# Optimization experiments

Hardware: AMD Instinct MI355X
Metric: run time of the kernel (lower is better)

The kernel has to match this reference:

```python
import jax, jax.numpy as jnp
import numpy as np

B, C3, H3, W3 = 8, 512, 24, 24
C5, H5, W5 = 256, 96, 96
GRIDS = (6, 3, 2, 1)
GROUPS = 2


def conv2d(x, w):
    # stride-1 'same' conv (matches torch autopad k//2 for odd k), NCHW/OIHW
    return jax.lax.conv_general_dilated(x, w, (1, 1), 'SAME',
                                        dimension_numbers=('NCHW', 'OIHW', 'NCHW'))


def conv_bn_silu(x, w):
    # ultralytics-style Conv = Conv2d(bias=False) + BatchNorm2d + SiLU.
    # BN in eval with default running stats (mean=0, var=1, gamma=1, beta=0) is identity.
    return jax.nn.silu(conv2d(x, w))


def psp(x):
    # adaptive_avg_pool2d to (g, g) for each grid; H,W divisible by all grids -> equal bins
    b, c, h, w = x.shape
    outs = []
    for g in GRIDS:
        outs.append(x.reshape(b, c, g, h // g, g, w // g).mean(axis=(3, 5)).reshape(b, c, g * g))
    return jnp.concatenate(outs, axis=2)  # [b, c, 36+9+4+1=50]


def resize_bilinear_ac(x, oh, ow):
    # F.interpolate(mode='bilinear', align_corners=True)
    n, c, h, w = x.shape
    ys = jnp.linspace(0.0, h - 1.0, oh)
    xs = jnp.linspace(0.0, w - 1.0, ow)
    y0 = jnp.clip(jnp.floor(ys).astype(jnp.int32), 0, h - 2)
    x0 = jnp.clip(jnp.floor(xs).astype(jnp.int32), 0, w - 2)
    wy = (ys - y0)[None, None, :, None]
    wx = (xs - x0)[None, None, None, :]
    xr = jnp.take(x, y0, axis=2) * (1 - wy) + jnp.take(x, y0 + 1, axis=2) * wy
    return jnp.take(xr, x0, axis=3) * (1 - wx) + jnp.take(xr, x0 + 1, axis=3) * wx


def grid_sample(img, grid):
    # F.grid_sample bilinear, align_corners=True, padding_mode='zeros'
    # img [N,C,H,W], grid [N,Ho,Wo,2] with (x,y) normalized coords
    n, c, h, w = img.shape
    gx = (grid[..., 0] + 1.0) * 0.5 * (w - 1)
    gy = (grid[..., 1] + 1.0) * 0.5 * (h - 1)
    x0 = jnp.floor(gx)
    y0 = jnp.floor(gy)
    wx1 = gx - x0
    wy1 = gy - y0
    flat = img.reshape(n, c, h * w)

    def gather(xi, yi, wgt):
        valid = (xi >= 0) & (xi <= w - 1) & (yi >= 0) & (yi <= h - 1)
        xc = jnp.clip(xi, 0, w - 1).astype(jnp.int32)
        yc = jnp.clip(yi, 0, h - 1).astype(jnp.int32)
        idx = (yc * w + xc).reshape(n, 1, -1)
        v = jnp.take_along_axis(flat, idx, axis=2).reshape(n, c, grid.shape[1], grid.shape[2])
        return v * (wgt * valid)[:, None]

    return (gather(x0, y0, (1 - wx1) * (1 - wy1)) + gather(x0 + 1, y0, wx1 * (1 - wy1))
            + gather(x0, y0 + 1, (1 - wx1) * wy1) + gather(x0 + 1, y0 + 1, wx1 * wy1))


def _w(key, shape):
    fan_in = int(np.prod(shape[1:]))
    return (jax.random.normal(key, shape, jnp.float32) / np.sqrt(fan_in)).astype(jnp.float32)


def setup_inputs() -> dict:
    key = jax.random.key(0)
    ks = jax.random.split(key, 17)
    return {
        'p3': jax.random.normal(ks[0], (B, C3, H3, W3), jnp.float32),
        'p5': jax.random.normal(ks[1], (B, C5, H5, W5), jnp.float32),
        # CFC_CRB
        'w_red': _w(ks[2], (C3, C3, 3, 3)),
        'wq': _w(ks[3], (32, C3, 1, 1)), 'bq': jnp.zeros((32,), jnp.float32),
        'wk': _w(ks[4], (32, C3)), 'bk': jnp.zeros((32,), jnp.float32),
        'wv': _w(ks[5], (C3, C3)), 'bv': jnp.zeros((C3,), jnp.float32),
        'la_w1': _w(ks[6], (C3 // 8, C3, 1, 1)),
        'la_w2': _w(ks[7], (C3, C3 // 8, 3, 3)),
        # SFC_G2
        'w32': _w(ks[8], (C5, C3, 3, 3)),
        'w8': _w(ks[9], (C5, C5, 3, 3)),
        'woff1': _w(ks[10], (64, 2 * C5, 1, 1)),
        'woff2': _w(ks[11], (GROUPS * 4 + 2, 64, 3, 3)),
    }


def reference(p3, p5, w_red, wq, bq, wk, bk, wv, bv, la_w1, la_w2, w32, w8, woff1, woff2):
    # ---------------- CFC_CRB ----------------
    x = conv_bn_silu(p3, w_red)                      # [b,512,h,w]
    b, c, h, w = x.shape
    q = conv2d(x, wq) + bq[None, :, None, None]       # [b,32,h,w]
    q = q.reshape(b, 32, h * w).transpose(0, 2, 1)    # [b,N,32]
    kfeat = psp(x)                                    # [b,512,50]
    k = jnp.einsum('oc,bcm->bom', wk, kfeat) + bk[None, :, None]   # [b,32,50]
    sim = jax.nn.softmax(jnp.einsum('bnc,bcm->bnm', q, k), axis=-1)  # [b,N,50]
    v = jnp.einsum('oc,bcm->bom', wv, kfeat) + bv[None, :, None]   # [b,512,50]
    context = jnp.einsum('bcm,bnm->bcn', v, sim).reshape(b, c, h, w)
    # LocalAttenModule: res1 * tanh(conv(context)) + res2
    mask = jnp.tanh(conv2d(conv_bn_silu(context, la_w1), la_w2))
    context = context * mask + context
    p3o = x + context                                 # [b,512,24,24]

    # ---------------- SFC_G2 ----------------
    sp = conv_bn_silu(p3o, w32)                       # [b,256,24,24]
    sp = resize_bilinear_ac(sp, H5, W5)               # [b,256,96,96]
    cp = conv_bn_silu(p5, w8)                         # [b,256,96,96]
    cr = conv2d(conv_bn_silu(jnp.concatenate([cp, sp], axis=1), woff1), woff2)  # [b,10,96,96]

    n = b
    spg = sp.reshape(n * GROUPS, -1, H5, W5)
    cpg = cp.reshape(n * GROUPS, -1, H5, W5)
    off_l = cr[:, 0:GROUPS * 2].reshape(n * GROUPS, 2, H5, W5)
    off_h = cr[:, GROUPS * 2:GROUPS * 4].reshape(n * GROUPS, 2, H5, W5)

    gx = jnp.linspace(-1.0, 1.0, W5)
    gy = jnp.linspace(-1.0, 1.0, H5)
    X, Y = jnp.meshgrid(gx, gy)                       # [H5,W5] each
    base = jnp.stack([X, Y], axis=-1)[None]           # [1,H5,W5,2] (x,y)
    norm = jnp.array([W5, H5], dtype=sp.dtype)
    grid_l = base + off_l.transpose(0, 2, 3, 1) / norm
    grid_h = base + off_h.transpose(0, 2, 3, 1) / norm

    cps = grid_sample(cpg, grid_l).reshape(n, -1, H5, W5)
    sps = grid_sample(spg, grid_h).reshape(n, -1, H5, W5)
    att = 1.0 + jnp.tanh(cr[:, GROUPS * 4:])          # [b,2,H,W]
    p5o = sps * att[:, 0:1] + cps * att[:, 1:2]
    return (p3o, p5o)
```

## Files before the change

kernel.cpp:

```cpp
#include <hip/hip_runtime.h>
#include <math.h>

#define DI __device__ __forceinline__

typedef __attribute__((ext_vector_type(8))) short bf16x8;
typedef __attribute__((ext_vector_type(4))) float f32x4;

DI float silu_f(float v) { return v / (1.f + __expf(-v)); }
DI float4 ld4(const float* p) { return *reinterpret_cast<const float4*>(p); }
DI void st4(float* p, const float4& v) { *reinterpret_cast<float4*>(p) = v; }
DI unsigned short f2bf(float f) {
    unsigned u = __float_as_uint(f);
    unsigned r = (u + 0x7FFFu + ((u >> 16) & 1u)) >> 16;
    return (unsigned short)r;
}
DI float bf2f(unsigned short u) { return __uint_as_float(((unsigned)u) << 16); }

DI void gload_lds16(const unsigned short* g, unsigned short* l) {
    __builtin_amdgcn_global_load_lds(
        (const __attribute__((address_space(1))) void*)g,
        (__attribute__((address_space(3))) void*)l, 16, 0, 0);
}

__global__ void pack_w2_kernel(const float* __restrict__ w, unsigned short* __restrict__ pk,
                               int Ci, int Co, int COG) {
    int idx = blockIdx.x * 256 + threadIdx.x;
    int total = Ci * Co * 9;
    if (idx >= total) return;
    int cc = idx & 31;
    int t = idx >> 5;
    int col = t % COG; t /= COG;
    int dydx = t % 9;  t /= 9;
    int nCoG = Co / COG;
    int cog = t % nCoG;
    int ch = t / nCoG;
    int co = cog * COG + col;
    pk[idx] = f2bf(w[((size_t)co * Ci + (ch << 5) + cc) * 9 + dydx]);
}

__global__ void pack_w1_kernel(const float* __restrict__ w, unsigned short* __restrict__ pk) {
    int idx = blockIdx.x * 256 + threadIdx.x;
    if (idx >= 32768) return;
    int cc = idx & 31;
    int col = (idx >> 5) & 63;
    int ch = idx >> 11;
    pk[idx] = f2bf(w[(size_t)col * 512 + (ch << 5) + cc]);
}

__global__ void pack_in_pad_kernel(const float* __restrict__ in, unsigned short* __restrict__ pk,
                                   int Ci, int H, int W, int total) {
    int idx = blockIdx.x * 256 + threadIdx.x;
    if (idx >= total) return;
    const int nCh = Ci >> 5;
    const int HW = H * W;
    int cg = idx & 3;
    int t = idx >> 2;
    int pix = t % HW; t /= HW;
    int ch = t % nCh;
    int b = t / nCh;
    int y = pix / W, x = pix % W;
    const float* src = in + ((size_t)b * Ci + (ch << 5) + (cg << 3)) * HW + pix;
    unsigned p[4];
#pragma unroll
    for (int j = 0; j < 4; ++j) {
        float v0 = src[(size_t)(2 * j) * HW];
        float v1 = src[(size_t)(2 * j + 1) * HW];
        p[j] = (unsigned)f2bf(v0) | ((unsigned)f2bf(v1) << 16);
    }
    size_t dst = (((size_t)b * nCh + ch) * (H + 2) + (y + 1)) * (W + 2) + (x + 1);
    *(uint4*)&pk[dst * 32 + (cg << 3)] = make_uint4(p[0], p[1], p[2], p[3]);
}

template <int TH, int TW, int BF, int WCO, int FUSE, int OUTPK, int OUTPAD>
__global__ void __launch_bounds__(256)
conv3x3_mfma3(const unsigned short* __restrict__ pin, const unsigned short* __restrict__ wpk,
              float* __restrict__ out, unsigned short* __restrict__ outpk,
              int B, int Ci, int Co, int H, int W,
              const float* __restrict__ ctx, const float* __restrict__ xres) {
    static_assert(TH * TW == 4 * BF * 16, "tile px = 4 waves * BF frags * 16");
    constexpr int COG = WCO * 16;
    constexpr int TWH = TW + 2;
    constexpr int HP = (TH + 2) * TWH;
    constexpr int NG = HP * 4;
    constexpr int NIT = (NG + 255) / 256;
    static_assert(NG % 8 == 0, "granules divisible by 8");
    __shared__ __align__(16) unsigned short linA[NG * 8];

    const int nTx = W / TW, nTy = H / TH, nCoG = Co / COG;
    const int Wp = W + 2, Hp = H + 2;
    const int nwg = gridDim.x;
    int wg = (blockIdx.x & 7) * (nwg >> 3) + (blockIdx.x >> 3);
    const int cog = wg % nCoG; wg /= nCoG;
    const int tx = wg % nTx;   wg /= nTx;
    const int ty = wg % nTy;
    const int b = wg / nTy;
    const int ox = tx * TW, oy = ty * TH, co0 = cog * COG;

    const int tid = threadIdx.x;
    const int lane = tid & 63;
    const int l15 = lane & 15, g = lane >> 4;
    const int wpx = (tid >> 6) * (BF * 16);

    int rr[BF], cc_[BF];
#pragma unroll
    for (int bf = 0; bf < BF; ++bf) {
        int px = wpx + bf * 16 + l15;
        rr[bf] = px / TW;
        cc_[bf] = px % TW;
    }

    f32x4 acc[WCO][BF];
#pragma unroll
    for (int af = 0; af < WCO; ++af)
#pragma unroll
        for (int bf = 0; bf < BF; ++bf) acc[af][bf] = {};

    const int nCh = Ci >> 5;
    const size_t HWs = (size_t)H * W;

    for (int ch = 0; ch < nCh; ++ch) {
        {
            const unsigned short* srcb =
                pin + ((size_t)b * nCh + ch) * (size_t)Hp * Wp * 32;
#pragma unroll
            for (int it = 0; it < NIT; ++it) {
                int s = it * 256 + tid;
                if (s < NG) {
                    int e = s ^ ((s >> 3) & 7);
                    int hp = e >> 2, cgp = e & 3;
                    int hy = hp / TWH, hx = hp - hy * TWH;
                    gload_lds16(srcb + ((size_t)(oy + hy) * Wp + (ox + hx)) * 32
                                     + (cgp << 3),
                                &linA[(s & ~63) << 3]);
                }
            }
        }
        __syncthreads();

        {
            const unsigned short* wbase =
                wpk + ((((size_t)ch * nCoG + cog) * 9) * COG + l15) * 32 + (g << 3);
#pragma unroll
            for (int dy = 0; dy < 3; ++dy) {
#pragma unroll
                for (int dx = 0; dx < 3; ++dx) {
                    const int dydx = dy * 3 + dx;
                    bf16x8 a[WCO];
#pragma unroll
                    for (int af = 0; af < WCO; ++af)
                        a[af] = *(const bf16x8*)(wbase + ((size_t)dydx * COG + af * 16) * 32);
                    bf16x8 bb[BF];
#pragma unroll
                    for (int bf = 0; bf < BF; ++bf) {
                        int pxh = (rr[bf] + dy) * TWH + cc_[bf] + dx;
                        int eg = (pxh << 2) | g;
                        int slot = eg ^ ((eg >> 3) & 7);
                        bb[bf] = *(const bf16x8*)&linA[slot << 3];
                    }
#pragma unroll
                    for (int af = 0; af < WCO; ++af)
#pragma unroll
                        for (int bf = 0; bf < BF; ++bf)
                            acc[af][bf] = __builtin_amdgcn_mfma_f32_16x16x32_bf16(
                                a[af], bb[bf], acc[af][bf], 0, 0, 0);
                }
            }
        }
        __syncthreads();
    }

    const int nChO = Co >> 5;
    const size_t opitch = OUTPAD ? (size_t)(H + 2) * (W + 2) : HWs;
#pragma unroll
    for (int af = 0; af < WCO; ++af) {
#pragma unroll
        for (int bf = 0; bf < BF; ++bf) {
            int px = wpx + bf * 16 + l15;
            int y = oy + px / TW, x = ox + px % TW;
            size_t pixg = (size_t)y * W + x;
            int coB = co0 + af * 16 + (g << 2);
            float vv[4];
#pragma unroll
            for (int r4 = 0; r4 < 4; ++r4) {
                float v = acc[af][bf][r4];
                if (FUSE == 1) v = silu_f(v);
                else if (FUSE == 2) {
                    size_t base = ((size_t)b * Co + coB + r4) * HWs + pixg;
                    v = xres[base] + ctx[base] * (1.f + tanhf(v));
                }
                vv[r4] = v;
            }
            if (OUTPK != 1) {
#pragma unroll
                for (int r4 = 0; r4 < 4; ++r4)
                    out[((size_t)b * Co + coB + r4) * HWs + pixg] = vv[r4];
            }
            if (OUTPK >= 1) {
                ushort4 s;
                s.x = f2bf(vv[0]); s.y = f2bf(vv[1]); s.z = f2bf(vv[2]); s.w = f2bf(vv[3]);
                size_t opix = OUTPAD ? ((size_t)(y + 1) * (W + 2) + (x + 1)) : pixg;
                *(ushort4*)&outpk[(((size_t)b * nChO + (coB >> 5)) * opitch + opix) * 32
                                  + (coB & 31)] = s;
            }
        }
    }
}

__global__ void __launch_bounds__(256)
cat_mfma(const unsigned short* __restrict__ cp_pk, const unsigned short* __restrict__ sp_pk,
         const unsigned short* __restrict__ wpk, float* __restrict__ out) {
    __shared__ __align__(16) unsigned short lin1[128 * 36];
    const int nwg = gridDim.x;
    int wg = (blockIdx.x & 7) * (nwg >> 3) + (blockIdx.x >> 3);
    int mt = wg % 72;
    int b = wg / 72;
    int m0 = mt * 128;
    const int tid = threadIdx.x;
    const int wave = tid >> 6, lane = tid & 63;
    const int l15 = lane & 15, g = lane >> 4;
    const int wpx = wave * 32;

    f32x4 acc[4][2];
#pragma unroll
    for (int af = 0; af < 4; ++af)
#pragma unroll
        for (int bf = 0; bf < 2; ++bf) acc[af][bf] = {};

    for (int ch = 0; ch < 16; ++ch) {
        const unsigned short* src = (ch < 8)
            ? cp_pk + (((size_t)b * 8 + ch) * 9216 + m0) * 32
            : sp_pk + (((size_t)b * 8 + ch - 8) * 9216 + m0) * 32;
#pragma unroll
        for (int it = 0; it < 2; ++it) {
            int e = tid + it * 256;
            int px = e >> 2, cg = e & 3;
            *(uint4*)&lin1[px * 36 + (cg << 3)] = *(const uint4*)&src[px * 32 + (cg << 3)];
        }
        __syncthreads();
        const unsigned short* wb = wpk + ((size_t)ch * 64 + l15) * 32 + g * 8;
        bf16x8 a[4];
#pragma unroll
        for (int af = 0; af < 4; ++af)
            a[af] = *(const bf16x8*)(wb + (af * 16) * 32);
        bf16x8 bb[2];
#pragma unroll
        for (int bf = 0; bf < 2; ++bf)
            bb[bf] = *(const bf16x8*)&lin1[(wpx + bf * 16 + l15) * 36 + g * 8];
#pragma unroll
        for (int af = 0; af < 4; ++af)
#pragma unroll
            for (int bf = 0; bf < 2; ++bf)
                acc[af][bf] = __builtin_amdgcn_mfma_f32_16x16x32_bf16(
                    a[af], bb[bf], acc[af][bf], 0, 0, 0);
        __syncthreads();
    }
#pragma unroll
    for (int af = 0; af < 4; ++af) {
#pragma unroll
        for (int bf = 0; bf < 2; ++bf) {
            int m = m0 + wpx + bf * 16 + l15;
#pragma unroll
            for (int r4 = 0; r4 < 4; ++r4) {
                int o = af * 16 + (g << 2) + r4;
                out[((size_t)b * 64 + o) * 9216 + m] = silu_f(acc[af][bf][r4]);
            }
        }
    }
}

DI void gs_params(int x, int y, float ox, float oy, float4* w, int2* p) {
    const float S = 47.5f / 96.f;
    float px = x + ox * S;
    float py = y + oy * S;
    float fx0 = floorf(px), fy0 = floorf(py);
    float wx = px - fx0, wy = py - fy0;
    float vx0 = (fx0 >= 0.f && fx0 <= 95.f) ? 1.f : 0.f;
    float vx1 = (fx0 >= -1.f && fx0 <= 94.f) ? 1.f : 0.f;
    float vy0 = (fy0 >= 0.f && fy0 <= 95.f) ? 1.f : 0.f;
    float vy1 = (fy0 >= -1.f && fy0 <= 94.f) ? 1.f : 0.f;
    int x0 = (int)fminf(fmaxf(fx0, 0.f), 95.f);
    int x1 = (int)fminf(fmaxf(fx0 + 1.f, 0.f), 95.f);
    int y0 = (int)fminf(fmaxf(fy0, 0.f), 95.f);
    int y1 = (int)fminf(fmaxf(fy0 + 1.f, 0.f), 95.f);
    w->x = (1.f - wx) * (1.f - wy) * vx0 * vy0;
    w->y = wx * (1.f - wy) * vx1 * vy0;
    w->z = (1.f - wx) * wy * vx0 * vy1;
    w->w = wx * wy * vx1 * vy1;
    *p = make_int2(x0 | (x1 << 16), y0 | (y1 << 16));
}

template <int TH, int TW, int CO_BLK, int CO_T, int CIC, int FUSE>
__global__ void __launch_bounds__(576)
conv3x3_kernel(const float* __restrict__ in, const float* __restrict__ wgt,
               float* __restrict__ out, int B, int Ci, int Co, int H, int W,
               float4* __restrict__ wpar, int2* __restrict__ ipk,
               float2* __restrict__ attp) {
    constexpr int TWH = TW + 2;
    constexpr int TWP = TW + 3;
    constexpr int SPAT = TH * (TW / 4);
    __shared__ float lin[CIC][TH + 2][TWP];
    __shared__ float wls[CIC][9][CO_BLK];
    __shared__ float crs[10][TH * TW + 1];

    const int nTx = W / TW, nTy = H / TH;
    const int nCoG = (Co + CO_BLK - 1) / CO_BLK;
    int bid = blockIdx.x;
    const int cog = bid % nCoG; bid /= nCoG;
    const int tx = bid % nTx;   bid /= nTx;
    const int ty = bid % nTy;
    const int b = bid / nTy;
    const int ox = tx * TW, oy = ty * TH;
    const int co0 = cog * CO_BLK;

    const int tid = threadIdx.x;
    const int cot = tid / SPAT;
    const int sp = tid % SPAT;
    const int r = sp / (TW / 4);
    const int cg = sp % (TW / 4);

    float acc[4][4];
#pragma unroll
    for (int i = 0; i < 4; ++i)
#pragma unroll
        for (int j = 0; j < 4; ++j) acc[i][j] = 0.f;

    for (int ci0 = 0; ci0 < Ci; ci0 += CIC) {
        for (int e = tid; e < CIC * (TH + 2) * TWH; e += SPAT * CO_T) {
            int xx = e % TWH;
            int yy = (e / TWH) % (TH + 2);
            int cc = e / (TWH * (TH + 2));
            int gy = oy - 1 + yy, gx = ox - 1 + xx;
            float v = 0.f;
            if (gy >= 0 && gy < H && gx >= 0 && gx < W)
                v = in[(((size_t)b * Ci + ci0 + cc) * H + gy) * W + gx];
            lin[cc][yy][xx] = v;
        }
        for (int e = tid; e < CIC * 9 * CO_BLK; e += SPAT * CO_T) {
            int col = e % CO_BLK;
            int k = (e / CO_BLK) % 9;
            int cc = e / (CO_BLK * 9);
            int co = co0 + col;
            float v = 0.f;
            if (co < Co) v = wgt[((size_t)co * Ci + ci0 + cc) * 9 + k];
            wls[cc][k][col] = v;
        }
        __syncthreads();
#pragma unroll
        for (int cc = 0; cc < CIC; ++cc) {
            float v0[3][6];
#pragma unroll
            for (int ky = 0; ky < 3; ++ky)
#pragma unroll
                for (int u = 0; u < 6; ++u)
                    v0[ky][u] = lin[cc][r + ky][cg * 4 + u];
#pragma unroll
            for (int ky = 0; ky < 3; ++ky)
#pragma unroll
                for (int kx = 0; kx < 3; ++kx) {
                    const float4 w4 = ld4(&wls[cc][ky * 3 + kx][cot * 4]);
                    const float wv_[4] = {w4.x, w4.y, w4.z, w4.w};
#pragma unroll
                    for (int i = 0; i < 4; ++i)
#pragma unroll
                        for (int j = 0; j < 4; ++j)
                            acc[i][j] = fmaf(wv_[i], v0[ky][kx + j], acc[i][j]);
                }
        }
        __syncthreads();
    }
    if (FUSE == 3) {
#pragma unroll
        for (int i = 0; i < 4; ++i) {
            int co = co0 + cot * 4 + i;
            if (co >= 10) continue;
#pragma unroll
            for (int j = 0; j < 4; ++j)
                crs[co][r * TW + cg * 4 + j] = acc[i][j];
        }
        __syncthreads();
        for (int e = tid; e < TH * TW; e += SPAT * CO_T) {
            int xx = ox + (e % TW), yy = oy + (e / TW);
            int pixg = yy * 96 + xx;
            float4 w; int2 p;
#pragma unroll
            for (int g2 = 0; g2 < 2; ++g2) {
                gs_params(xx, yy, crs[2 * g2][e], crs[2 * g2 + 1][e], &w, &p);
                size_t el = ((size_t)g2 * 8 + b) * 9216 + pixg;
                wpar[el] = w; ipk[el] = p;
                gs_params(xx, yy, crs[4 + 2 * g2][e], crs[5 + 2 * g2][e], &w, &p);
                size_t eh = ((size_t)(2 + g2) * 8 + b) * 9216 + pixg;
                wpar[eh] = w; ipk[eh] = p;
            }
            float2 at;
            at.x = 1.f + tanhf(crs[8][e]);
            at.y = 1.f + tanhf(crs[9][e]);
            attp[(size_t)b * 9216 + pixg] = at;
        }
    } else {
        const int y = oy + r;
        const int xb = ox + cg * 4;
#pragma unroll
        for (int i = 0; i < 4; ++i) {
            int co = co0 + cot * 4 + i;
            if (co >= Co) continue;
            size_t base = (((size_t)b * Co + co) * H + y) * W + xb;
            float4 res;
            res.x = acc[i][0]; res.y = acc[i][1]; res.z = acc[i][2]; res.w = acc[i][3];
            st4(&out[base], res);
        }
    }
}

template <int ACT, int PK>
__global__ void __launch_bounds__(256)
gemm_om(const float* __restrict__ W, const float* __restrict__ bias,
        const float* __restrict__ in, float* __restrict__ out,
        unsigned short* __restrict__ pko,
        int B, int C, int O, int M, int nOt, int nMt) {
    __shared__ float xs[32][66];
    __shared__ float wls[64][33];
    int bid = blockIdx.x;
    int mt = bid % nMt; bid /= nMt;
    int ot = bid % nOt;
    int b  = bid / nOt;
    int o0 = ot * 64, m0 = mt * 64;
    int tid = threadIdx.x;
    int m_t = tid & 15, o_g = tid >> 4;
    float acc[4][4];
#pragma unroll
    for (int i = 0; i < 4; ++i)
#pragma unroll
        for (int j = 0; j < 4; ++j) acc[i][j] = 0.f;

    for (int c0 = 0; c0 < C; c0 += 32) {
#pragma unroll
        for (int it = 0; it < 8; ++it) {
            int e = tid + it * 256;
            int mm = e & 63, cc = e >> 6;
            float v = 0.f;
            if (m0 + mm < M) v = in[((size_t)b * C + c0 + cc) * M + m0 + mm];
            xs[cc][mm] = v;
        }
#pragma unroll
        for (int it = 0; it < 8; ++it) {
            int e = tid + it * 256;
            int cc = e & 31, ol = e >> 5;
            float v = 0.f;
            if (o0 + ol < O) v = W[(size_t)(o0 + ol) * C + c0 + cc];
            wls[ol][cc] = v;
        }
        __syncthreads();
#pragma unroll
        for (int cc = 0; cc < 32; ++cc) {
            float xv[4], wv[4];
#pragma unroll
            for (int j = 0; j < 4; ++j) xv[j] = xs[cc][j * 16 + m_t];
#pragma unroll
            for (int i = 0; i < 4; ++i) wv[i] = wls[o_g * 4 + i][cc];
#pragma unroll
            for (int i = 0; i < 4; ++i)
#pragma unroll
                for (int j = 0; j < 4; ++j)
                    acc[i][j] = fmaf(wv[i], xv[j], acc[i][j]);
        }
        __syncthreads();
    }
#pragma unroll
    for (int i = 0; i < 4; ++i) {
        int o = o0 + o_g * 4 + i;
        if (o >= O) continue;
        float bv = bias ? bias[o] : 0.f;
#pragma unroll
        for (int j = 0; j < 4; ++j) {
            int m = m0 + j * 16 + m_t;
            if (m >= M) continue;
            float v = acc[i][j] + bv;
            if (ACT == 1) v = silu_f(v);
            if (PK) {
                int yy = m / 24, xx = m % 24;
                pko[(((size_t)b * (O >> 5) + (o >> 5)) * 676
                     + (size_t)(yy + 1) * 26 + (xx + 1)) * 32 + (o & 31)] = f2bf(v);
            } else {
                out[((size_t)b * O + o) * M + m] = v;
            }
        }
    }
}

__global__ void psp_kernel(const float* __restrict__ x, float* __restrict__ kf) {
    __shared__ float pl[576];
    int bc = blockIdx.x;
    const float* xp = x + (size_t)bc * 576;
    for (int e = threadIdx.x; e < 576; e += 64) pl[e] = xp[e];
    __syncthreads();
    int m = threadIdx.x;
    if (m < 50) {
        int g, i0;
        if (m < 36)      { g = 6; i0 = m; }
        else if (m < 45) { g = 3; i0 = m - 36; }
        else if (m < 49) { g = 2; i0 = m - 45; }
        else             { g = 1; i0 = 0; }
        int bs = 24 / g;
        int by = i0 / g, bx = i0 % g;
        float s = 0.f;
        for (int yy = 0; yy < bs; ++yy)
            for (int xx = 0; xx < bs; ++xx)
                s += pl[(by * bs + yy) * 24 + bx * bs + xx];
        kf[(size_t)bc * 50 + m] = s / (float)(bs * bs);
    }
}

__global__ void __launch_bounds__(256)
sim_kernel(const float* __restrict__ q, const float* __restrict__ k,
           float* __restrict__ simg) {
    __shared__ float qs[32][65];
    __shared__ float ks[32][52];
    __shared__ float sm[64][52];
    int b = blockIdx.x / 9, n0 = (blockIdx.x % 9) * 64;
    int tid = threadIdx.x;
    for (int e = tid; e < 32 * 64; e += 256) {
        int c = e >> 6, n = e & 63;
        qs[c][n] = q[((size_t)b * 32 + c) * 576 + n0 + n];
    }
    for (int e = tid; e < 32 * 50; e += 256) {
        int c = e / 50, m = e % 50;
        ks[c][m] = k[((size_t)b * 32 + c) * 50 + m];
    }
    __syncthreads();
    for (int e = tid; e < 64 * 50; e += 256) {
        int n = e / 50, m = e % 50;
        float s = 0.f;
#pragma unroll
        for (int c = 0; c < 32; ++c) s = fmaf(qs[c][n], ks[c][m], s);
        sm[n][m] = s;
    }
    __syncthreads();
    if (tid < 64) {
        float mx = -1e30f;
        for (int m = 0; m < 50; ++m) mx = fmaxf(mx, sm[tid][m]);
        float sum = 0.f;
        for (int m = 0; m < 50; ++m) {
            float e2 = __expf(sm[tid][m] - mx);
            sm[tid][m] = e2;
            sum += e2;
        }
        float inv = 1.f / sum;
        for (int m = 0; m < 50; ++m) sm[tid][m] *= inv;
    }
    __syncthreads();
    for (int e = tid; e < 64 * 50; e += 256) {
        int n = e / 50, m = e % 50;
        simg[((size_t)b * 576 + n0 + n) * 50 + m] = sm[n][m];
    }
}

__global__ void __launch_bounds__(256)
ctx_kernel(const float* __restrict__ v, const float* __restrict__ simg,
           float* __restrict__ ctx) {
    __shared__ float vs[128][54];
    __shared__ float ss[64][54];
    int blk = blockIdx.x;
    int ct = blk & 3; blk >>= 2;
    int nt = blk % 9;
    int b = blk / 9;
    int c0 = ct * 128, n0 = nt * 64;
    int tid = threadIdx.x;
    for (int e = tid; e < 128 * 50; e += 256) {
        int c = e / 50, m = e % 50;
        vs[c][m] = v[((size_t)b * 512 + c0 + c) * 50 + m];
    }
    for (int e = tid; e < 64 * 50; e += 256) {
        int n = e / 50, m = e % 50;
        ss[n][m] = simg[((size_t)b * 576 + n0 + n) * 50 + m];
    }
    __syncthreads();
    int n_t = tid & 15;
    int c_t = tid >> 4;
    float acc[8][4];
#pragma unroll
    for (int i = 0; i < 8; ++i)
#pragma unroll
        for (int j = 0; j < 4; ++j) acc[i][j] = 0.f;
    for (int m = 0; m < 50; ++m) {
        float sv[4];
#pragma unroll
        for (int j = 0; j < 4; ++j) sv[j] = ss[j * 16 + n_t][m];
#pragma unroll
        for (int i = 0; i < 8; ++i) {
            float vv = vs[c_t * 8 + i][m];
#pragma unroll
            for (int j = 0; j < 4; ++j) acc[i][j] = fmaf(vv, sv[j], acc[i][j]);
        }
    }
#pragma unroll
    for (int i = 0; i < 8; ++i)
#pragma unroll
        for (int j = 0; j < 4; ++j)
            ctx[((size_t)b * 512 + c0 + c_t * 8 + i) * 576 + n0 + j * 16 + n_t] = acc[i][j];
}

__global__ void upsample2_kernel(const float* __restrict__ in, unsigned short* __restrict__ outpk) {
    int idx = blockIdx.x * 256 + threadIdx.x;
    if (idx >= 8 * 8 * 4 * 9216) return;
    int cg = idx & 3;
    int t = idx >> 2;
    int pix = t % 9216; t /= 9216;
    int ch = t & 7;
    int b = t >> 3;
    int x = pix % 96, y = pix / 96;
    float fy = y * (23.f / 95.f);
    float fx = x * (23.f / 95.f);
    int y0 = (int)fy; if (y0 > 22) y0 = 22;
    int x0 = (int)fx; if (x0 > 22) x0 = 22;
    float wy = fy - y0, wx = fx - x0;
    const float* base = in + ((size_t)b * 256 + ch * 32 + cg * 8) * 576 + y0 * 24 + x0;
    unsigned short s[8];
#pragma unroll
    for (int j = 0; j < 8; ++j) {
        const float* ip = base + (size_t)j * 576;
        float a = ip[0], bb = ip[1], c = ip[24], d = ip[25];
        float l = a * (1.f - wy) + c * wy;
        float r = bb * (1.f - wy) + d * wy;
        s[j] = f2bf(l * (1.f - wx) + r * wx);
    }
    *(uint4*)&outpk[(((size_t)b * 8 + ch) * 9216 + pix) * 32 + cg * 8] =
        make_uint4((unsigned)s[0] | ((unsigned)s[1] << 16),
                   (unsigned)s[2] | ((unsigned)s[3] << 16),
                   (unsigned)s[4] | ((unsigned)s[5] << 16),
                   (unsigned)s[6] | ((unsigned)s[7] << 16));
}

__global__ void __launch_bounds__(256)
gsample3_kernel(const unsigned short* __restrict__ cp_pk, const unsigned short* __restrict__ sp_pk,
                const float4* __restrict__ wpar, const int2* __restrict__ ipk,
                const float2* __restrict__ attp, float* __restrict__ p5o) {
    int idx = blockIdx.x * 256 + threadIdx.x;
    if (idx >= 8 * 32 * 9216) return;
    int pix = idx % 9216;
    int cb = (idx / 9216) & 31;
    int b = idx / (9216 * 32);
    int c0 = cb * 8;
    int g = c0 >> 7, ch = c0 >> 5, coff = c0 & 31;
    size_t el = ((size_t)g * 8 + b) * 9216 + pix;
    size_t eh = ((size_t)(2 + g) * 8 + b) * 9216 + pix;
    float4 wl = wpar[el]; int2 pl = ipk[el];
    float4 wh = wpar[eh]; int2 ph = ipk[eh];
    float2 at = attp[(size_t)b * 9216 + pix];
    int l00 = (pl.y & 0xffff) * 96 + (pl.x & 0xffff);
    int l01 = (pl.y & 0xffff) * 96 + (pl.x >> 16);
    int l10 = (pl.y >> 16) * 96 + (pl.x & 0xffff);
    int l11 = (pl.y >> 16) * 96 + (pl.x >> 16);
    int h00 = (ph.y & 0xffff) * 96 + (ph.x & 0xffff);
    int h01 = (ph.y & 0xffff) * 96 + (ph.x >> 16);
    int h10 = (ph.y >> 16) * 96 + (ph.x & 0xffff);
    int h11 = (ph.y >> 16) * 96 + (ph.x >> 16);
    const unsigned short* cb0 = cp_pk + (((size_t)b * 8 + ch) * 9216) * 32 + coff;
    const unsigned short* sb0 = sp_pk + (((size_t)b * 8 + ch) * 9216) * 32 + coff;
    ushort4 tc0 = *(const ushort4*)&cb0[(size_t)l00 * 32];
    ushort4 tc0b = *(const ushort4*)&cb0[(size_t)l00 * 32 + 4];
    ushort4 tc1 = *(const ushort4*)&cb0[(size_t)l01 * 32];
    ushort4 tc1b = *(const ushort4*)&cb0[(size_t)l01 * 32 + 4];
    ushort4 tc2 = *(const ushort4*)&cb0[(size_t)l10 * 32];
    ushort4 tc2b = *(const ushort4*)&cb0[(size_t)l10 * 32 + 4];
    ushort4 tc3 = *(const ushort4*)&cb0[(size_t)l11 * 32];
    ushort4 tc3b = *(const ushort4*)&cb0[(size_t)l11 * 32 + 4];
    ushort4 ts0 = *(const ushort4*)&sb0[(size_t)h00 * 32];
    ushort4 ts0b = *(const ushort4*)&sb0[(size_t)h00 * 32 + 4];
    ushort4 ts1 = *(const ushort4*)&sb0[(size_t)h01 * 32];
    ushort4 ts1b = *(const ushort4*)&sb0[(size_t)h01 * 32 + 4];
    ushort4 ts2 = *(const ushort4*)&sb0[(size_t)h10 * 32];
    ushort4 ts2b = *(const ushort4*)&sb0[(size_t)h10 * 32 + 4];
    ushort4 ts3 = *(const ushort4*)&sb0[(size_t)h11 * 32];
    ushort4 ts3b = *(const ushort4*)&sb0[(size_t)h11 * 32 + 4];
    const unsigned short* c0a = (const unsigned short*)&tc0;
    const unsigned short* c0bp = (const unsigned short*)&tc0b;
    const unsigned short* c1a = (const unsigned short*)&tc1;
    const unsigned short* c1bp = (const unsigned short*)&tc1b;
    const unsigned short* c2a = (const unsigned short*)&tc2;
    const unsigned short* c2bp = (const unsigned short*)&tc2b;
    const unsigned short* c3a = (const unsigned short*)&tc3;
    const unsigned short* c3bp = (const unsigned short*)&tc3b;
    const unsigned short* s0a = (const unsigned short*)&ts0;
    const unsigned short* s0bp = (const unsigned short*)&ts0b;
    const unsigned short* s1a = (const unsigned short*)&ts1;
    const unsigned short* s1bp = (const unsigned short*)&ts1b;
    const unsigned short* s2a = (const unsigned short*)&ts2;
    const unsigned short* s2bp = (const unsigned short*)&ts2b;
    const unsigned short* s3a = (const unsigned short*)&ts3;
    const unsigned short* s3bp = (const unsigned short*)&ts3b;
    float* op = p5o + ((size_t)b * 256 + c0) * 9216 + pix;
#pragma unroll
    for (int i = 0; i < 8; ++i) {
        unsigned short v0 = (i < 4) ? c0a[i] : c0bp[i - 4];
        unsigned short v1 = (i < 4) ? c1a[i] : c1bp[i - 4];
        unsigned short v2 = (i < 4) ? c2a[i] : c2bp[i - 4];
        unsigned short v3 = (i < 4) ? c3a[i] : c3bp[i - 4];
        float cps = wl.x * bf2f(v0) + wl.y * bf2f(v1) + wl.z * bf2f(v2) + wl.w * bf2f(v3);
        unsigned short u0 = (i < 4) ? s0a[i] : s0bp[i - 4];
        unsigned short u1 = (i < 4) ? s1a[i] : s1bp[i - 4];
        unsigned short u2 = (i < 4) ? s2a[i] : s2bp[i - 4];
        unsigned short u3 = (i < 4) ? s3a[i] : s3bp[i - 4];
        float sps = wh.x * bf2f(u0) + wh.y * bf2f(u1) + wh.z * bf2f(u2) + wh.w * bf2f(u3);
        op[(size_t)i * 9216] = sps * at.x + cps * at.y;
    }
}

extern "C" void kernel_launch(void* const* d_in, const int* in_sizes, int n_in,
                              void* d_out, int out_size, void* d_ws, size_t ws_size,
                              hipStream_t stream) {
    const float* p3    = (const float*)d_in[0];
    const float* p5    = (const float*)d_in[1];
    const float* w_red = (const float*)d_in[2];
    const float* wq    = (const float*)d_in[3];
    const float* bq    = (const float*)d_in[4];
    const float* wk    = (const float*)d_in[5];
    const float* bk    = (const float*)d_in[6];
    const float* wv    = (const float*)d_in[7];
    const float* bv    = (const float*)d_in[8];
    const float* la_w1 = (const float*)d_in[9];
    const float* la_w2 = (const float*)d_in[10];
    const float* w32   = (const float*)d_in[11];
    const float* w8    = (const float*)d_in[12];
    const float* woff1 = (const float*)d_in[13];
    const float* woff2 = (const float*)d_in[14];

    float* out = (float*)d_out;
    float* p3o = out;
    float* p5o = out + 2359296;

    float* ws = (float*)d_ws;
    float* x_   = ws + 0;
    float* ctx  = ws + 2359296;
    float* q    = ws + 4718592;
    float* kf   = ws + 4866048;
    float* km   = ws + 5070848;
    float* vm   = ws + 5083648;
    unsigned short* la1_pk = (unsigned short*)(ws + 5288448);
    float* sp24 = ws + 5461504;
    float4* wpar = (float4*)(ws + 6641152);
    int2*   ipk  = (int2*)(ws + 7820800);
    float2* attp = (float2*)(ws + 8410624);
    float* simg = ws + 8558080;
    unsigned short* sp96_pk = (unsigned short*)(ws + 8788480);
    unsigned short* cp_pk   = (unsigned short*)(ws + 18225664);
    unsigned short* p5_pk   = (unsigned short*)(ws + 27662848);
    unsigned short* p3_pk   = (unsigned short*)(ws + 37497344);
    unsigned short* wred_pk = (unsigned short*)(ws + 38881792);
    unsigned short* w32_pk  = (unsigned short*)(ws + 40061440);
    unsigned short* w8_pk   = (unsigned short*)(ws + 40651264);
    unsigned short* wla2_pk = (unsigned short*)(ws + 40946176);
    unsigned short* woff1_pk= (unsigned short*)(ws + 41093632);
    float* t64  = ws + 0;

    hipMemsetAsync(p5_pk, 0, (size_t)8 * 8 * 98 * 98 * 32 * 2, stream);
    hipMemsetAsync(p3_pk, 0, (size_t)8 * 16 * 676 * 32 * 2, stream);
    hipMemsetAsync(la1_pk, 0, (size_t)8 * 2 * 676 * 32 * 2, stream);

    pack_w2_kernel<<<dim3(2359296 / 256), dim3(256), 0, stream>>>(w_red, wred_pk, 512, 512, 32);
    pack_w2_kernel<<<dim3(1179648 / 256), dim3(256), 0, stream>>>(w32, w32_pk, 512, 256, 16);
    pack_w2_kernel<<<dim3(589824 / 256), dim3(256), 0, stream>>>(w8, w8_pk, 256, 256, 64);
    pack_w2_kernel<<<dim3(294912 / 256), dim3(256), 0, stream>>>(la_w2, wla2_pk, 64, 512, 32);
    pack_w1_kernel<<<dim3(128), dim3(256), 0, stream>>>(woff1, woff1_pk);
    pack_in_pad_kernel<<<dim3(9216), dim3(256), 0, stream>>>(p5, p5_pk, 256, 96, 96, 2359296);
    pack_in_pad_kernel<<<dim3(1152), dim3(256), 0, stream>>>(p3, p3_pk, 512, 24, 24, 294912);

    conv3x3_mfma3<16, 16, 4, 4, 1, 1, 0><<<dim3(1152), dim3(256), 0, stream>>>(
        p5_pk, w8_pk, nullptr, cp_pk, 8, 256, 256, 96, 96, nullptr, nullptr);
    conv3x3_mfma3<8, 24, 3, 2, 1, 0, 0><<<dim3(384), dim3(256), 0, stream>>>(
        p3_pk, wred_pk, x_, nullptr, 8, 512, 512, 24, 24, nullptr, nullptr);
    gemm_om<0, 0><<<dim3(72), dim3(256), 0, stream>>>(
        wq, bq, x_, q, nullptr, 8, 512, 32, 576, 1, 9);
    psp_kernel<<<dim3(8 * 512), dim3(64), 0, stream>>>(x_, kf);
    gemm_om<0, 0><<<dim3(8), dim3(256), 0, stream>>>(
        wk, bk, kf, km, nullptr, 8, 512, 32, 50, 1, 1);
    gemm_om<0, 0><<<dim3(64), dim3(256), 0, stream>>>(
        wv, bv, kf, vm, nullptr, 8, 512, 512, 50, 8, 1);
    sim_kernel<<<dim3(72), dim3(256), 0, stream>>>(q, km, simg);
    ctx_kernel<<<dim3(288), dim3(256), 0, stream>>>(vm, simg, ctx);
    gemm_om<1, 1><<<dim3(72), dim3(256), 0, stream>>>(
        la_w1, nullptr, ctx, nullptr, la1_pk, 8, 512, 64, 576, 1, 9);
    conv3x3_mfma3<8, 24, 3, 2, 2, 2, 1><<<dim3(384), dim3(256), 0, stream>>>(
        la1_pk, wla2_pk, p3o, p3_pk, 8, 64, 512, 24, 24, ctx, x_);
    conv3x3_mfma3<8, 24, 3, 1, 1, 0, 0><<<dim3(384), dim3(256), 0, stream>>>(
        p3_pk, w32_pk, sp24, nullptr, 8, 512, 256, 24, 24, nullptr, nullptr);
    upsample2_kernel<<<dim3(9216), dim3(256), 0, stream>>>(sp24, sp96_pk);
    cat_mfma<<<dim3(576), dim3(256), 0, stream>>>(cp_pk, sp96_pk, woff1_pk, t64);
    conv3x3_kernel<8, 32, 12, 3, 4, 3><<<dim3(288), dim3(192), 0, stream>>>(
        t64, woff2, nullptr, 8, 64, 10, 96, 96, wpar, ipk, attp);
    gsample3_kernel<<<dim3(9216), dim3(256), 0, stream>>>(
        cp_pk, sp96_pk, wpar, ipk, attp, p5o);
}
```

Before: 857.3 us.

## Drop LDS staging in 3x3 MFMA conv and read activations directly from global

The conv kernel no longer stages each input halo tile into shared memory with async global-to-LDS loads and two barriers per channel chunk. Each lane now loads its B fragments straight from the padded packed input in global memory at every tap. This removes the barriers and the LDS footprint, which can raise occupancy. In exchange it repeats up to nine overlapping global or L1/L2 reads per pixel and loses the overlap the async copy gave.

```diff
diff --git a/kernel.cpp b/kernel.cpp
--- a/kernel.cpp
+++ b/kernel.cpp
@@ -15,12 +15,6 @@
     return (unsigned short)r;
 }
 DI float bf2f(unsigned short u) { return __uint_as_float(((unsigned)u) << 16); }
-
-DI void gload_lds16(const unsigned short* g, unsigned short* l) {
-    __builtin_amdgcn_global_load_lds(
-        (const __attribute__((address_space(1))) void*)g,
-        (__attribute__((address_space(3))) void*)l, 16, 0, 0);
-}
 
 __global__ void pack_w2_kernel(const float* __restrict__ w, unsigned short* __restrict__ pk,
                                int Ci, int Co, int COG) {
@@ -73,18 +67,12 @@
 
 template <int TH, int TW, int BF, int WCO, int FUSE, int OUTPK, int OUTPAD>
 __global__ void __launch_bounds__(256)
-conv3x3_mfma3(const unsigned short* __restrict__ pin, const unsigned short* __restrict__ wpk,
+conv3x3_mfma4(const unsigned short* __restrict__ pin, const unsigned short* __restrict__ wpk,
               float* __restrict__ out, unsigned short* __restrict__ outpk,
               int B, int Ci, int Co, int H, int W,
               const float* __restrict__ ctx, const float* __restrict__ xres) {
     static_assert(TH * TW == 4 * BF * 16, "tile px = 4 waves * BF frags * 16");
     constexpr int COG = WCO * 16;
-    constexpr int TWH = TW + 2;
-    constexpr int HP = (TH + 2) * TWH;
-    constexpr int NG = HP * 4;
-    constexpr int NIT = (NG + 255) / 256;
-    static_assert(NG % 8 == 0, "granules divisible by 8");
-    __shared__ __align__(16) unsigned short linA[NG * 8];
 
     const int nTx = W / TW, nTy = H / TH, nCoG = Co / COG;
     const int Wp = W + 2, Hp = H + 2;
@@ -101,12 +89,11 @@
     const int l15 = lane & 15, g = lane >> 4;
     const int wpx = (tid >> 6) * (BF * 16);
 
-    int rr[BF], cc_[BF];
+    int pixoff[BF];
 #pragma unroll
     for (int bf = 0; bf < BF; ++bf) {
         int px = wpx + bf * 16 + l15;
-        rr[bf] = px / TW;
-        cc_[bf] = px % TW;
+        pixoff[bf] = (oy + px / TW) * Wp + (ox + px % TW);
     }
 
     f32x4 acc[WCO][BF];
@@ -117,56 +104,33 @@
 
     const int nCh = Ci >> 5;
     const size_t HWs = (size_t)H * W;
+    const size_t HpWp = (size_t)Hp * Wp;
 
     for (int ch = 0; ch < nCh; ++ch) {
-        {
-            const unsigned short* srcb =
-                pin + ((size_t)b * nCh + ch) * (size_t)Hp * Wp * 32;
-#pragma unroll
-            for (int it = 0; it < NIT; ++it) {
-                int s = it * 256 + tid;
-                if (s < NG) {
-                    int e = s ^ ((s >> 3) & 7);
-                    int hp = e >> 2, cgp = e & 3;
-                    int hy = hp / TWH, hx = hp - hy * TWH;
-                    gload_lds16(srcb + ((size_t)(oy + hy) * Wp + (ox + hx)) * 32
-                                     + (cgp << 3),
-                                &linA[(s & ~63) << 3]);
-                }
+        const unsigned short* srcb = pin + ((size_t)b * nCh + ch) * HpWp * 32 + (g << 3);
+        const unsigned short* wbase =
+            wpk + ((((size_t)ch * nCoG + cog) * 9) * COG + l15) * 32 + (g << 3);
+#pragma unroll
+        for (int dy = 0; dy < 3; ++dy) {
+#pragma unroll
+            for (int dx = 0; dx < 3; ++dx) {
+                const int dydx = dy * 3 + dx;
+                bf16x8 a[WCO];
+#pragma unroll
+                for (int af = 0; af < WCO; ++af)
+                    a[af] = *(const bf16x8*)(wbase + ((size_t)dydx * COG + af * 16) * 32);
+                bf16x8 bb[BF];
+#pragma unroll
+                for (int bf = 0; bf < BF; ++bf)
+                    bb[bf] = *(const bf16x8*)(srcb + (size_t)(pixoff[bf] + dy * Wp + dx) * 32);
+#pragma unroll
+                for (int af = 0; af < WCO; ++af)
+#pragma unroll
+                    for (int bf = 0; bf < BF; ++bf)
+                        acc[af][bf] = __builtin_amdgcn_mfma_f32_16x16x32_bf16(
+                            a[af], bb[bf], acc[af][bf], 0, 0, 0);
             }
         }
-        __syncthreads();
-
-        {
-            const unsigned short* wbase =
-                wpk + ((((size_t)ch * nCoG + cog) * 9) * COG + l15) * 32 + (g << 3);
-#pragma unroll
-            for (int dy = 0; dy < 3; ++dy) {
-#pragma unroll
-                for (int dx = 0; dx < 3; ++dx) {
-                    const int dydx = dy * 3 + dx;
-                    bf16x8 a[WCO];
-#pragma unroll
-                    for (int af = 0; af < WCO; ++af)
-                        a[af] = *(const bf16x8*)(wbase + ((size_t)dydx * COG + af * 16) * 32);
-                    bf16x8 bb[BF];
-#pragma unroll
-                    for (int bf = 0; bf < BF; ++bf) {
-                        int pxh = (rr[bf] + dy) * TWH + cc_[bf] + dx;
-                        int eg = (pxh << 2) | g;
-                        int slot = eg ^ ((eg >> 3) & 7);
-                        bb[bf] = *(const bf16x8*)&linA[slot << 3];
-                    }
-#pragma unroll
-                    for (int af = 0; af < WCO; ++af)
-#pragma unroll
-                        for (int bf = 0; bf < BF; ++bf)
-                            acc[af][bf] = __builtin_amdgcn_mfma_f32_16x16x32_bf16(
-                                a[af], bb[bf], acc[af][bf], 0, 0, 0);
-                }
-            }
-        }
-        __syncthreads();
     }
 
     const int nChO = Co >> 5;
@@ -764,9 +728,9 @@
     pack_in_pad_kernel<<<dim3(9216), dim3(256), 0, stream>>>(p5, p5_pk, 256, 96, 96, 2359296);
     pack_in_pad_kernel<<<dim3(1152), dim3(256), 0, stream>>>(p3, p3_pk, 512, 24, 24, 294912);
 
-    conv3x3_mfma3<16, 16, 4, 4, 1, 1, 0><<<dim3(1152), dim3(256), 0, stream>>>(
+    conv3x3_mfma4<16, 16, 4, 4, 1, 1, 0><<<dim3(1152), dim3(256), 0, stream>>>(
         p5_pk, w8_pk, nullptr, cp_pk, 8, 256, 256, 96, 96, nullptr, nullptr);
-    conv3x3_mfma3<8, 24, 3, 2, 1, 0, 0><<<dim3(384), dim3(256), 0, stream>>>(
+    conv3x3_mfma4<8, 24, 3, 2, 1, 0, 0><<<dim3(384), dim3(256), 0, stream>>>(
         p3_pk, wred_pk, x_, nullptr, 8, 512, 512, 24, 24, nullptr, nullptr);
     gemm_om<0, 0><<<dim3(72), dim3(256), 0, stream>>>(
         wq, bq, x_, q, nullptr, 8, 512, 32, 576, 1, 9);
@@ -779,9 +743,9 @@
     ctx_kernel<<<dim3(288), dim3(256), 0, stream>>>(vm, simg, ctx);
     gemm_om<1, 1><<<dim3(72), dim3(256), 0, stream>>>(
         la_w1, nullptr, ctx, nullptr, la1_pk, 8, 512, 64, 576, 1, 9);
-    conv3x3_mfma3<8, 24, 3, 2, 2, 2, 1><<<dim3(384), dim3(256), 0, stream>>>(
+    conv3x3_mfma4<8, 24, 3, 2, 2, 2, 1><<<dim3(384), dim3(256), 0, stream>>>(
         la1_pk, wla2_pk, p3o, p3_pk, 8, 64, 512, 24, 24, ctx, x_);
-    conv3x3_mfma3<8, 24, 3, 1, 1, 0, 0><<<dim3(384), dim3(256), 0, stream>>>(
+    conv3x3_mfma4<8, 24, 3, 1, 1, 0, 0><<<dim3(384), dim3(256), 0, stream>>>(
         p3_pk, w32_pk, sp24, nullptr, 8, 512, 256, 24, 24, nullptr, nullptr);
     upsample2_kernel<<<dim3(9216), dim3(256), 0, stream>>>(sp24, sp96_pk);
     cat_mfma<<<dim3(576), dim3(256), 0, stream>>>(cp_pk, sp96_pk, woff1_pk, t64);
```

After: 1.079 ms. 25.8% more time.
